# Kernel optimization log

Measured on AMD Instinct MI355X. Metric: run time of the kernel, lower is better.

Reference implementation:

```python
import jax, jax.numpy as jnp
import numpy as np

ATTN_DIM = 256


def setup_inputs() -> dict:
    key = jax.random.key(0)
    ks = jax.random.split(key, 10)
    B, Cu, Cj, H, W = 4, 320, 1024, 64, 64
    return {
        "unet_feat": jax.random.normal(ks[0], (B, Cu, H, W), jnp.float32),
        "janus_feat": jax.random.normal(ks[1], (B, Cj, H, W), jnp.float32),
        "Wq": jax.random.normal(ks[2], (ATTN_DIM, Cu), jnp.float32) * 0.02,
        "bq": jnp.zeros((ATTN_DIM,), jnp.float32),
        "Wk": jax.random.normal(ks[3], (ATTN_DIM, Cj), jnp.float32) * 0.02,
        "bk": jnp.zeros((ATTN_DIM,), jnp.float32),
        "Wv": jax.random.normal(ks[4], (Cu, Cj), jnp.float32) * 0.02,
        "bv": jnp.zeros((Cu,), jnp.float32),
        "Wo": jax.random.normal(ks[5], (Cu, Cu), jnp.float32) * 0.02,
        "bo": jnp.zeros((Cu,), jnp.float32),
    }


def reference(unet_feat, janus_feat, Wq, bq, Wk, bk, Wv, bv, Wo, bo):
    B, Cu, H, W = unet_feat.shape
    scale = ATTN_DIM ** (-0.5)
    # 1x1 convs == channel matmuls
    q = jnp.einsum('oc,bchw->bohw', Wq, unet_feat) + bq[None, :, None, None]
    k = jnp.einsum('oc,bchw->bohw', Wk, janus_feat) + bk[None, :, None, None]
    v = jnp.einsum('oc,bchw->bohw', Wv, janus_feat) + bv[None, :, None, None]
    N = H * W
    q = q.reshape(B, ATTN_DIM, N).transpose(0, 2, 1)  # [B, N, C]
    k = k.reshape(B, ATTN_DIM, N)                     # [B, C, N]
    v = v.reshape(B, Cu, N)                           # [B, Cu, N]
    attn = jax.nn.softmax(jnp.einsum('bic,bcj->bij', q, k) * scale, axis=-1)
    out = jnp.einsum('bcj,bij->bci', v, attn)         # [B, Cu, N]
    out = out.reshape(B, Cu, H, W)
    out = jnp.einsum('oc,bchw->bohw', Wo, out) + bo[None, :, None, None]
    return unet_feat + out
```

## Files before the change

kernel.cpp:

```cpp
#include <hip/hip_runtime.h>
#include <hip/hip_bf16.h>
#include <math.h>


typedef unsigned short u16;
typedef __attribute__((ext_vector_type(8))) short bf16x8;
typedef __attribute__((ext_vector_type(4))) float f32x4;
typedef __attribute__((ext_vector_type(16))) float f32x16;
typedef __attribute__((ext_vector_type(4))) unsigned short u16x4;

#define NB 4
#define CU 320
#define CJ 1024
#define NN 4096
#define AD 256

#define XU_OFF 0u
#define XJ_OFF 10485760u
#define QB_OFF 44040192u
#define KB_OFF 52428800u
#define VB_OFF 60817408u
#define WQ_OFF 71303168u
#define WK_OFF 71467008u
#define WV_OFF 71991296u
#define WO_OFF 72646656u
#define AO_OFF XU_OFF

__device__ __forceinline__ u16 f2b(float f) {
    union { float f; unsigned u; } v; v.f = f;
    unsigned u = v.u;
    unsigned r = (u + 0x7fffu + ((u >> 16) & 1u)) >> 16;
    return (u16)r;
}

__device__ __forceinline__ float b2f(u16 x) {
    union { unsigned u; float f; } v; v.u = ((unsigned)x) << 16;
    return v.f;
}

__device__ __forceinline__ unsigned cvt_pk_bf16(float lo, float hi) {
    unsigned r;
    asm("v_cvt_pk_bf16_f32 %0, %1, %2" : "=v"(r) : "v"(lo), "v"(hi));
    return r;
}

__device__ __forceinline__ float exp2_fast(float x) {
    float r;
    asm("v_exp_f32 %0, %1" : "=v"(r) : "v"(x));
    return r;
}

__device__ __forceinline__ void async_cp16(const u16* g, char* l) {
    __builtin_amdgcn_global_load_lds(
        (const __attribute__((address_space(1))) unsigned int*)g,
        (__attribute__((address_space(3))) unsigned int*)l, 16, 0, 0);
}

__global__ void wcast_kernel(const float* __restrict__ Wq, const float* __restrict__ Wk,
                             const float* __restrict__ Wv, const float* __restrict__ Wo,
                             u16* __restrict__ wq, u16* __restrict__ wk,
                             u16* __restrict__ wv, u16* __restrict__ wo) {
    int id = blockIdx.x * 256 + threadIdx.x;
    if (id < 81920) { wq[id] = f2b(Wq[id]); return; }
    id -= 81920;
    if (id < 262144) { wk[id] = f2b(Wk[id]); return; }
    id -= 262144;
    if (id < 327680) { wv[id] = f2b(Wv[id]); return; }
    id -= 327680;
    if (id < 102400) { wo[id] = f2b(Wo[id]); }
}

__global__ __launch_bounds__(256) void transpose_cast_kernel(
        const float* __restrict__ in, u16* __restrict__ out, int C, int Nn) {
    __shared__ float tile[64][65];
    int b = blockIdx.z;
    int n0 = blockIdx.x * 64, c0 = blockIdx.y * 64;
    const float* src = in + (size_t)b * C * Nn;
    u16* dst = out + (size_t)b * Nn * C;
    int t = threadIdx.x;
    int nl = t & 63, cl = t >> 6;
    #pragma unroll
    for (int k = 0; k < 16; ++k) {
        int c = cl + k * 4;
        tile[c][nl] = src[(size_t)(c0 + c) * Nn + n0 + nl];
    }
    __syncthreads();
    int cl2 = t & 63, nl2 = t >> 6;
    #pragma unroll
    for (int k = 0; k < 16; ++k) {
        int n = nl2 + k * 4;
        dst[(size_t)(n0 + n) * C + c0 + cl2] = f2b(tile[cl2][n]);
    }
}

template <int EPI, int KD, int NOUT>
__global__ __launch_bounds__(256, 2) void gemm_kernel(
        const u16* __restrict__ A, const u16* __restrict__ W,
        const float* __restrict__ bias, void* __restrict__ outp,
        const float* __restrict__ unet, float alpha) {
    __shared__ __align__(16) char smem[49152];
    const int t = threadIdx.x;
    const int lane = t & 63, wave = t >> 6;
    const int r = lane & 15, h = lane >> 4;
    const int wr = wave >> 1, wc = wave & 1;
    const int m0 = blockIdx.x * 128;
    const int bn0 = blockIdx.y * 64;

    int goffA[4], goffB[2];
    #pragma unroll
    for (int n = 0; n < 4; ++n) {
        int c = n * 256 + t;
        int row = c >> 3, s = c & 7;
        goffA[n] = (m0 + row) * KD + ((s ^ (row & 7)) << 3);
    }
    #pragma unroll
    for (int n = 0; n < 2; ++n) {
        int c = n * 256 + t;
        int row = c >> 3, s = c & 7;
        goffB[n] = (bn0 + row) * KD + ((s ^ (row & 7)) << 3);
    }
    const unsigned wb = (unsigned)(t & ~63) * 16u;

    #define GSTAGE(BUF, KT) do {                                                  \
        _Pragma("unroll")                                                         \
        for (int n_ = 0; n_ < 4; ++n_)                                            \
            async_cp16(A + goffA[n_] + (KT) * 64,                                 \
                       smem + (BUF) * 24576 + n_ * 4096 + wb);                    \
        _Pragma("unroll")                                                         \
        for (int n_ = 0; n_ < 2; ++n_)                                            \
            async_cp16(W + goffB[n_] + (KT) * 64,                                 \
                       smem + (BUF) * 24576 + 16384 + n_ * 4096 + wb);            \
    } while (0)

    f32x4 acc[4][2];
    #pragma unroll
    for (int fr = 0; fr < 4; ++fr)
        #pragma unroll
        for (int fc = 0; fc < 2; ++fc) acc[fr][fc] = (f32x4)0.0f;

    GSTAGE(0, 0);
    int buf = 0;
    const int KS = KD / 64;
    for (int kt = 0; kt < KS; ++kt) {
        if (kt < KS - 1) {
            GSTAGE(buf ^ 1, kt + 1);
            asm volatile("s_waitcnt vmcnt(6)" ::: "memory");
        } else {
            asm volatile("s_waitcnt vmcnt(0)" ::: "memory");
        }
        __builtin_amdgcn_s_barrier();
        asm volatile("" ::: "memory");
        const char* Ab = smem + buf * 24576;
        const char* Bb = smem + buf * 24576 + 16384;
        #pragma unroll
        for (int kk = 0; kk < 2; ++kk) {
            bf16x8 af[4], bf[2];
            #pragma unroll
            for (int fr = 0; fr < 4; ++fr) {
                int row = wr * 64 + fr * 16 + r;
                af[fr] = *(const bf16x8*)(Ab + row * 128 + (((kk * 4 + h) ^ (row & 7)) << 4));
            }
            #pragma unroll
            for (int fc = 0; fc < 2; ++fc) {
                int rowb = wc * 32 + fc * 16 + r;
                bf[fc] = *(const bf16x8*)(Bb + rowb * 128 + (((kk * 4 + h) ^ (rowb & 7)) << 4));
            }
            #pragma unroll
            for (int fr = 0; fr < 4; ++fr)
                #pragma unroll
                for (int fc = 0; fc < 2; ++fc)
                    acc[fr][fc] = __builtin_amdgcn_mfma_f32_16x16x32_bf16(
                        af[fr], bf[fc], acc[fr][fc], 0, 0, 0);
        }
        asm volatile("" ::: "memory");
        __builtin_amdgcn_s_barrier();
        asm volatile("" ::: "memory");
        buf ^= 1;
    }
    #undef GSTAGE

    const int mw = m0 + wr * 64;
    const int ob0 = bn0 + wc * 32;

    if (EPI == 0) {
        u16* out = (u16*)outp;
        #pragma unroll
        for (int fc = 0; fc < 2; ++fc) {
            int o = ob0 + fc * 16 + r;
            float bs = bias[o];
            #pragma unroll
            for (int fr = 0; fr < 4; ++fr)
                #pragma unroll
                for (int rr = 0; rr < 4; ++rr) {
                    int mrow = mw + fr * 16 + h * 4 + rr;
                    out[(size_t)mrow * NOUT + o] = f2b((acc[fr][fc][rr] + bs) * alpha);
                }
        }
    } else {
        float* tile = (float*)(smem + wave * 8704);
        #pragma unroll
        for (int fc = 0; fc < 2; ++fc)
            #pragma unroll
            for (int fr = 0; fr < 4; ++fr)
                *(f32x4*)(tile + (fc * 16 + r) * 68 + fr * 16 + h * 4) = acc[fr][fc];
        __builtin_amdgcn_s_waitcnt(0);
        float* out = (float*)outp;
        int bb = mw >> 12, nb = mw & 4095;
        #pragma unroll
        for (int g = 0; g < 8; ++g) {
            int chunk = g * 64 + lane;
            int row = chunk >> 4, ns = chunk & 15;
            int o = ob0 + row;
            size_t base = (size_t)bb * CU * NN + (size_t)o * NN + nb + ns * 4;
            f32x4 v = *(const f32x4*)(tile + row * 68 + ns * 4);
            f32x4 u = *(const f32x4*)(unet + base);
            float bs = bias[o];
            f32x4 res;
            #pragma unroll
            for (int rr = 0; rr < 4; ++rr) res[rr] = v[rr] + bs + u[rr];
            *(f32x4*)(out + base) = res;
        }
    }
}

__global__ __launch_bounds__(256, 2) void gemm_kv_kernel(
        const u16* __restrict__ A, const u16* __restrict__ Wk,
        const u16* __restrict__ Wv, const float* __restrict__ bk,
        const float* __restrict__ bv, u16* __restrict__ Kb,
        u16* __restrict__ Vb) {
    const int KD = 1024;
    __shared__ __align__(16) char smem[49152];
    const int t = threadIdx.x;
    const int lane = t & 63, wave = t >> 6;
    const int r = lane & 15, h = lane >> 4;
    const int wr = wave >> 1, wc = wave & 1;
    const int m0 = blockIdx.x * 128;
    const bool isK = blockIdx.y < 4;
    const int bn0 = (isK ? blockIdx.y : (blockIdx.y - 4)) * 64;
    const u16* W = isK ? Wk : Wv;
    const float* bias = isK ? bk : bv;

    int goffA[4], goffB[2];
    #pragma unroll
    for (int n = 0; n < 4; ++n) {
        int c = n * 256 + t;
        int row = c >> 3, s = c & 7;
        goffA[n] = (m0 + row) * KD + ((s ^ (row & 7)) << 3);
    }
    #pragma unroll
    for (int n = 0; n < 2; ++n) {
        int c = n * 256 + t;
        int row = c >> 3, s = c & 7;
        goffB[n] = (bn0 + row) * KD + ((s ^ (row & 7)) << 3);
    }
    const unsigned wb = (unsigned)(t & ~63) * 16u;

    #define GSTAGE(BUF, KT) do {                                                  \
        _Pragma("unroll")                                                         \
        for (int n_ = 0; n_ < 4; ++n_)                                            \
            async_cp16(A + goffA[n_] + (KT) * 64,                                 \
                       smem + (BUF) * 24576 + n_ * 4096 + wb);                    \
        _Pragma("unroll")                                                         \
        for (int n_ = 0; n_ < 2; ++n_)                                            \
            async_cp16(W + goffB[n_] + (KT) * 64,                                 \
                       smem + (BUF) * 24576 + 16384 + n_ * 4096 + wb);            \
    } while (0)

    f32x4 acc[4][2];
    #pragma unroll
    for (int fr = 0; fr < 4; ++fr)
        #pragma unroll
        for (int fc = 0; fc < 2; ++fc) acc[fr][fc] = (f32x4)0.0f;

    GSTAGE(0, 0);
    int buf = 0;
    for (int kt = 0; kt < 16; ++kt) {
        if (kt < 15) {
            GSTAGE(buf ^ 1, kt + 1);
            asm volatile("s_waitcnt vmcnt(6)" ::: "memory");
        } else {
            asm volatile("s_waitcnt vmcnt(0)" ::: "memory");
        }
        __builtin_amdgcn_s_barrier();
        asm volatile("" ::: "memory");
        const char* Ab = smem + buf * 24576;
        const char* Bb = smem + buf * 24576 + 16384;
        #pragma unroll
        for (int kk = 0; kk < 2; ++kk) {
            bf16x8 af[4], bf[2];
            #pragma unroll
            for (int fr = 0; fr < 4; ++fr) {
                int row = wr * 64 + fr * 16 + r;
                af[fr] = *(const bf16x8*)(Ab + row * 128 + (((kk * 4 + h) ^ (row & 7)) << 4));
            }
            #pragma unroll
            for (int fc = 0; fc < 2; ++fc) {
                int rowb = wc * 32 + fc * 16 + r;
                bf[fc] = *(const bf16x8*)(Bb + rowb * 128 + (((kk * 4 + h) ^ (rowb & 7)) << 4));
            }
            #pragma unroll
            for (int fr = 0; fr < 4; ++fr)
                #pragma unroll
                for (int fc = 0; fc < 2; ++fc)
                    acc[fr][fc] = __builtin_amdgcn_mfma_f32_16x16x32_bf16(
                        af[fr], bf[fc], acc[fr][fc], 0, 0, 0);
        }
        asm volatile("" ::: "memory");
        __builtin_amdgcn_s_barrier();
        asm volatile("" ::: "memory");
        buf ^= 1;
    }
    #undef GSTAGE

    const int mw = m0 + wr * 64;
    const int ob0 = bn0 + wc * 32;

    if (isK) {
        #pragma unroll
        for (int fc = 0; fc < 2; ++fc) {
            int o = ob0 + fc * 16 + r;
            float bs = bias[o];
            #pragma unroll
            for (int fr = 0; fr < 4; ++fr)
                #pragma unroll
                for (int rr = 0; rr < 4; ++rr) {
                    int mrow = mw + fr * 16 + h * 4 + rr;
                    Kb[(size_t)mrow * AD + o] = f2b((acc[fr][fc][rr] + bs));
                }
        }
    } else {
        u16* tile = (u16*)(smem + wave * 4608);
        #pragma unroll
        for (int fc = 0; fc < 2; ++fc) {
            int o = ob0 + fc * 16 + r;
            float bs = bias[o];
            #pragma unroll
            for (int fr = 0; fr < 4; ++fr) {
                u16x4 v4;
                #pragma unroll
                for (int rr = 0; rr < 4; ++rr) v4[rr] = f2b(acc[fr][fc][rr] + bs);
                *(u16x4*)(tile + (fc * 16 + r) * 72 + fr * 16 + h * 4) = v4;
            }
        }
        __builtin_amdgcn_s_waitcnt(0);
        int bb = mw >> 12, nb = mw & 4095;
        #pragma unroll
        for (int g = 0; g < 4; ++g) {
            int chunk = g * 64 + lane;
            int row = chunk >> 3, ns = chunk & 7;
            int ch = ob0 + row;
            int j = nb + ns * 8;
            bf16x8 val = *(const bf16x8*)(tile + row * 72 + ns * 8);
            size_t off = (size_t)bb * CU * NN + (size_t)(ch >> 5) * (NN * 32)
                       + (size_t)(j >> 4) * 512
                       + (size_t)((ch & 31) + ((j >> 3) & 1) * 32) * 8 + (j & 7);
            *(bf16x8*)(Vb + off) = val;
        }
    }
}

__global__ __launch_bounds__(768, 3) void attn_kernel(
        const u16* __restrict__ Q, const u16* __restrict__ K,
        const u16* __restrict__ V, u16* __restrict__ AO) {
    __shared__ __align__(16) char smem[84480];

    const int t = threadIdx.x;
    const int lane = t & 63;
    const int wave = t >> 6;
    const int r = lane & 31, hi = lane >> 5;

    int linear = blockIdx.x;
    int swz = (linear & 7) * 32 + (linear >> 3);
    int b = swz >> 6;
    int i0 = (swz & 63) * 64;

    const u16* Qb = Q + ((size_t)b * NN + i0) * AD;
    const u16* Kb = K + (size_t)b * NN * AD;
    const u16* Vb = V + (size_t)b * CU * NN;

    {
        #pragma unroll
        for (int n = 0; n < 2; ++n) {
            int id = n * 768 + t;
            int row = (id >> 5) & 63, c16 = id & 31;
            async_cp16(Kb + row * 256 + ((c16 ^ (row & 31)) << 3),
                       smem + (unsigned)(n * 768 + (t & ~63)) * 16u);
        }
        if (t < 512) {
            int id = 1536 + t;
            int row = (id >> 5) & 63, c16 = id & 31;
            async_cp16(Kb + row * 256 + ((c16 ^ (row & 31)) << 3),
                       smem + (unsigned)(1536 + (t & ~63)) * 16u);
        }
    }
    asm volatile("s_waitcnt vmcnt(0)" ::: "memory");
    __builtin_amdgcn_s_barrier();
    asm volatile("" ::: "memory");

    if (wave < 4) {
        const int iw = wave >> 1;
        const int jw = wave & 1;
        bf16x8 q[16];
        #pragma unroll
        for (int kk = 0; kk < 16; ++kk)
            q[kk] = *(const bf16x8*)(Qb + (size_t)(iw * 32 + r) * AD + kk * 16 + hi * 8);
        float m = -INFINITY, lsum = 0.0f;

        for (int i = 0; i < 64; ++i) {
            if (i) {
                __builtin_amdgcn_s_barrier();
                asm volatile("" ::: "memory");
            }
            const char* Kt = smem + (i & 1) * 32768 + jw * 16384;
            f32x16 sa = (f32x16)0.0f, sb = (f32x16)0.0f;
            __builtin_amdgcn_s_setprio(1);
            #pragma unroll
            for (int kk = 0; kk < 8; ++kk) {
                bf16x8 k0 = *(const bf16x8*)(Kt + r * 512 + (((2 * kk + hi) ^ r) << 4));
                bf16x8 k1 = *(const bf16x8*)(Kt + r * 512 + (((2 * (kk + 8) + hi) ^ r) << 4));
                sa = __builtin_amdgcn_mfma_f32_32x32x16_bf16(k0, q[kk], sa, 0, 0, 0);
                sb = __builtin_amdgcn_mfma_f32_32x32x16_bf16(k1, q[kk + 8], sb, 0, 0, 0);
            }
            __builtin_amdgcn_s_setprio(0);
            f32x16 s = sa + sb;

            float x0 = fmaxf(s[0], s[1]),   x1 = fmaxf(s[2], s[3]);
            float x2 = fmaxf(s[4], s[5]),   x3 = fmaxf(s[6], s[7]);
            float x4 = fmaxf(s[8], s[9]),   x5 = fmaxf(s[10], s[11]);
            float x6 = fmaxf(s[12], s[13]), x7 = fmaxf(s[14], s[15]);
            float pmax = fmaxf(fmaxf(fmaxf(x0, x1), fmaxf(x2, x3)),
                               fmaxf(fmaxf(x4, x5), fmaxf(x6, x7)));
            pmax = fmaxf(pmax, __shfl_xor(pmax, 32));
            char* pb = smem + 65536 + (i & 1) * 8960;
            int fl = __any(pmax > m + 8.0f) ? 1 : 0;
            if (fl) {
                float mn = fmaxf(m, pmax);
                float al = exp2_fast(m - mn);
                m = mn;
                lsum *= al;
                if (lane < 32) *(float*)(pb + 8192 + (iw * 2 + jw) * 128 + r * 4) = al;
            }
            if (lane == 0) *(int*)(pb + 8704 + (iw * 2 + jw) * 4) = fl;
            float p[16];
            #pragma unroll
            for (int e = 0; e < 16; ++e) p[e] = exp2_fast(s[e] - m);
            float y0 = (p[0] + p[1]) + (p[2] + p[3]);
            float y1 = (p[4] + p[5]) + (p[6] + p[7]);
            float y2 = (p[8] + p[9]) + (p[10] + p[11]);
            float y3 = (p[12] + p[13]) + (p[14] + p[15]);
            float ps = (y0 + y1) + (y2 + y3);
            ps += __shfl_xor(ps, 32);
            lsum += ps;

            #pragma unroll
            for (int ks = 0; ks < 2; ++ks) {
                unsigned a0 = cvt_pk_bf16(p[8 * ks + 0], p[8 * ks + 1]);
                unsigned a1 = cvt_pk_bf16(p[8 * ks + 2], p[8 * ks + 3]);
                unsigned b0 = cvt_pk_bf16(p[8 * ks + 4], p[8 * ks + 5]);
                unsigned b1 = cvt_pk_bf16(p[8 * ks + 6], p[8 * ks + 7]);
                asm("v_permlane32_swap_b32 %0, %1" : "+v"(a0), "+v"(b0));
                asm("v_permlane32_swap_b32 %0, %1" : "+v"(a1), "+v"(b1));
                union { unsigned w[4]; bf16x8 v; } u;
                u.w[0] = a0; u.w[1] = a1; u.w[2] = b0; u.w[3] = b1;
                *(bf16x8*)(pb + (iw * 2 + jw) * 2048 + ks * 1024 + lane * 16) = u.v;
            }
            asm volatile("s_waitcnt lgkmcnt(0)" ::: "memory");
            __builtin_amdgcn_sched_barrier(0);
        }
        __builtin_amdgcn_s_barrier();
        asm volatile("" ::: "memory");
        if (lane < 32) {
            *(float*)(smem + 83456 + (iw * 2 + jw) * 128 + r * 4) = m;
            *(float*)(smem + 83456 + 512 + (iw * 2 + jw) * 128 + r * 4) = lsum;
        }
        __syncthreads();
        __syncthreads();
        __syncthreads();
    } else {
        const int pvid = wave - 4;
        const int iw = pvid >> 2;
        const int pj = (pvid >> 1) & 1;
        const int cgh = pvid & 1;
        const int tp = t - 256;

        int goffp[4];
        #pragma unroll
        for (int n = 0; n < 4; ++n) {
            int id = n * 512 + tp;
            int row = (id >> 5) & 63;
            int c16 = id & 31;
            goffp[n] = row * 256 + ((c16 ^ (row & 31)) << 3);
        }
        const unsigned wbp = (unsigned)(tp & ~63) * 16u;

        #define STAGE(BUF, KP) do {                                               \
            _Pragma("unroll")                                                     \
            for (int n_ = 0; n_ < 4; ++n_)                                        \
                async_cp16((KP) + goffp[n_],                                      \
                           smem + (BUF) * 32768 + n_ * 8192 + wbp);               \
        } while (0)

        f32x16 o[5];
        #pragma unroll
        for (int ct = 0; ct < 5; ++ct) o[ct] = (f32x16)0.0f;
        const u16* vb = Vb + (size_t)(cgh * 5) * 131072 + lane * 8;

        #define PV_BODY(TI) do {                                                  \
            const char* pb = smem + 65536 + ((TI) & 1) * 8960;                    \
            int fl = *(volatile const int*)(pb + 8704 + (iw * 2 + pj) * 4);       \
            bf16x8 pf0 = *(const bf16x8*)(pb + (iw * 2 + pj) * 2048 + lane * 16); \
            bf16x8 pf1 = *(const bf16x8*)(pb + (iw * 2 + pj) * 2048 + 1024 +      \
                                          lane * 16);                             \
            bf16x8 vfA[5], vfB[5];                                                \
            _Pragma("unroll")                                                     \
            for (int c = 0; c < 5; ++c)                                           \
                vfA[c] = *(const bf16x8*)(vb + (size_t)c * 131072 +               \
                                          ((TI) * 4 + pj * 2 + 0) * 512);         \
            _Pragma("unroll")                                                     \
            for (int c = 0; c < 5; ++c)                                           \
                vfB[c] = *(const bf16x8*)(vb + (size_t)c * 131072 +               \
                                          ((TI) * 4 + pj * 2 + 1) * 512);         \
            if (fl) {                                                             \
                float alv = *(volatile const float*)(pb + 8192 +                  \
                                (iw * 2 + pj) * 128 + (lane & 31) * 4);           \
                _Pragma("unroll")                                                 \
                for (int ct = 0; ct < 5; ++ct) o[ct] *= alv;                      \
            }                                                                     \
            __builtin_amdgcn_s_setprio(1);                                        \
            _Pragma("unroll")                                                     \
            for (int ct = 0; ct < 5; ++ct)                                        \
                o[ct] = __builtin_amdgcn_mfma_f32_32x32x16_bf16(vfA[ct], pf0,     \
                                                                o[ct], 0, 0, 0); \
            _Pragma("unroll")                                                     \
            for (int ct = 0; ct < 5; ++ct)                                        \
                o[ct] = __builtin_amdgcn_mfma_f32_32x32x16_bf16(vfB[ct], pf1,     \
                                                                o[ct], 0, 0, 0); \
            __builtin_amdgcn_s_setprio(0);                                        \
        } while (0)

        for (int i = 0; i < 64; ++i) {
            if (i) {
                __builtin_amdgcn_s_barrier();
                asm volatile("" ::: "memory");
            }
            if (i < 63) STAGE((i + 1) & 1, Kb + (i + 1) * 16384);
            if (i >= 1) PV_BODY(i - 1);
            asm volatile("s_waitcnt vmcnt(0)" ::: "memory");
        }
        __builtin_amdgcn_s_barrier();
        asm volatile("" ::: "memory");
        PV_BODY(63);

        __syncthreads();
        float m0 = *(const float*)(smem + 83456 + (iw * 2 + pj) * 128 + r * 4);
        float l0 = *(const float*)(smem + 83456 + 512 + (iw * 2 + pj) * 128 + r * 4);
        float m1 = *(const float*)(smem + 83456 + (iw * 2 + (pj ^ 1)) * 128 + r * 4);
        float l1 = *(const float*)(smem + 83456 + 512 + (iw * 2 + (pj ^ 1)) * 128 + r * 4);
        float M = fmaxf(m0, m1);
        float fsc = exp2_fast(m0 - M);
        float fo = exp2_fast(m1 - M);
        float inv = 1.0f / (l0 * fsc + l1 * fo);

        u16* fb = (u16*)smem;
        if (pj == 1) {
            #pragma unroll
            for (int ct = 0; ct < 5; ++ct)
                #pragma unroll
                for (int e = 0; e < 16; ++e) {
                    int c = cgh * 160 + ct * 32 + (e & 3) + 8 * (e >> 2) + 4 * hi;
                    fb[(iw * 32 + r) * 328 + c] = f2b(o[ct][e] * fsc);
                }
        }
        __syncthreads();
        if (pj == 0) {
            #pragma unroll
            for (int ct = 0; ct < 5; ++ct)
                #pragma unroll
                for (int g = 0; g < 4; ++g) {
                    int cb = cgh * 160 + ct * 32 + 8 * g + 4 * hi;
                    u16* fr = &fb[(iw * 32 + r) * 328 + cb];
                    float v0 = (o[ct][4 * g + 0] * fsc + b2f(fr[0])) * inv;
                    float v1 = (o[ct][4 * g + 1] * fsc + b2f(fr[1])) * inv;
                    float v2 = (o[ct][4 * g + 2] * fsc + b2f(fr[2])) * inv;
                    float v3 = (o[ct][4 * g + 3] * fsc + b2f(fr[3])) * inv;
                    *(unsigned*)(fr) = cvt_pk_bf16(v0, v1);
                    *(unsigned*)(fr + 2) = cvt_pk_bf16(v2, v3);
                }
        }
        __syncthreads();
        #undef PV_BODY
        #undef STAGE
    }

    const u16* ob = (const u16*)smem;
    u16* AOb = AO + ((size_t)b * NN + i0) * CU;
    #pragma unroll
    for (int n = 0; n < 3; ++n) {
        int id = n * 768 + t;
        int row = id / 40, c8 = id % 40;
        bf16x8 val = *(const bf16x8*)(ob + row * 328 + c8 * 8);
        *(bf16x8*)(AOb + (size_t)row * CU + c8 * 8) = val;
    }
    if (t < 256) {
        int id = 2304 + t;
        int row = id / 40, c8 = id % 40;
        bf16x8 val = *(const bf16x8*)(ob + row * 328 + c8 * 8);
        *(bf16x8*)(AOb + (size_t)row * CU + c8 * 8) = val;
    }
}

extern "C" void kernel_launch(void* const* d_in, const int* in_sizes, int n_in,
                              void* d_out, int out_size, void* d_ws, size_t ws_size,
                              hipStream_t stream) {
    const float* unet  = (const float*)d_in[0];
    const float* janus = (const float*)d_in[1];
    const float* Wq = (const float*)d_in[2];
    const float* bq = (const float*)d_in[3];
    const float* Wk = (const float*)d_in[4];
    const float* bk = (const float*)d_in[5];
    const float* Wv = (const float*)d_in[6];
    const float* bv = (const float*)d_in[7];
    const float* Wo = (const float*)d_in[8];
    const float* bo = (const float*)d_in[9];
    float* out = (float*)d_out;

    char* ws = (char*)d_ws;
    u16* Xu  = (u16*)(ws + XU_OFF);
    u16* Xj  = (u16*)(ws + XJ_OFF);
    u16* Qb  = (u16*)(ws + QB_OFF);
    u16* Kb  = (u16*)(ws + KB_OFF);
    u16* Vb  = (u16*)(ws + VB_OFF);
    u16* wq  = (u16*)(ws + WQ_OFF);
    u16* wk  = (u16*)(ws + WK_OFF);
    u16* wv  = (u16*)(ws + WV_OFF);
    u16* wo  = (u16*)(ws + WO_OFF);
    u16* AO  = (u16*)(ws + AO_OFF);

    wcast_kernel<<<3024, 256, 0, stream>>>(Wq, Wk, Wv, Wo, wq, wk, wv, wo);

    transpose_cast_kernel<<<dim3(64, 5, NB), 256, 0, stream>>>(unet, Xu, CU, NN);
    transpose_cast_kernel<<<dim3(64, 16, NB), 256, 0, stream>>>(janus, Xj, CJ, NN);

    gemm_kernel<0, 320, 256><<<dim3(128, 4), 256, 0, stream>>>(
        Xu, wq, bq, Qb, nullptr, 0.0901684411f);

    gemm_kv_kernel<<<dim3(128, 9), 256, 0, stream>>>(
        Xj, wk, wv, bk, bv, Kb, Vb);

    attn_kernel<<<256, 768, 0, stream>>>(Qb, Kb, Vb, AO);

    gemm_kernel<2, 320, 320><<<dim3(128, 5), 256, 0, stream>>>(
        AO, wo, bo, out, unet, 1.0f);
}
```

Before: 183.7 us.

## Repartition attention PV waves to share V fragments across row tiles

The attention block grows from 12 to 14 waves, giving 10 PV waves instead of 8. Each PV wave now covers both 32-row query tiles and two 32-channel V tiles, rather than one row tile and five channel tiles. Each V fragment loaded from global memory then feeds two MFMAs, roughly halving per-block V load traffic and lowering accumulator registers per wave. The K staging, output copy and launch bounds are adjusted to the new thread count. In exchange, the extra waves add P fragment reads from LDS and scheduling pressure, and two waves sit idle during K staging.

```diff
diff --git a/kernel.cpp b/kernel.cpp
--- a/kernel.cpp
+++ b/kernel.cpp
@@ -359,7 +359,7 @@
     }
 }
 
-__global__ __launch_bounds__(768, 3) void attn_kernel(
+__global__ __launch_bounds__(896, 3) void attn_kernel(
         const u16* __restrict__ Q, const u16* __restrict__ K,
         const u16* __restrict__ V, u16* __restrict__ AO) {
     __shared__ __align__(16) char smem[84480];
@@ -381,16 +381,18 @@
     {
         #pragma unroll
         for (int n = 0; n < 2; ++n) {
-            int id = n * 768 + t;
+            int id = n * 896 + t;
+            if (id < 2048) {
+                int row = (id >> 5) & 63, c16 = id & 31;
+                async_cp16(Kb + row * 256 + ((c16 ^ (row & 31)) << 3),
+                           smem + (unsigned)(n * 896 + (t & ~63)) * 16u);
+            }
+        }
+        if (t < 256) {
+            int id = 1792 + t;
             int row = (id >> 5) & 63, c16 = id & 31;
             async_cp16(Kb + row * 256 + ((c16 ^ (row & 31)) << 3),
-                       smem + (unsigned)(n * 768 + (t & ~63)) * 16u);
-        }
-        if (t < 512) {
-            int id = 1536 + t;
-            int row = (id >> 5) & 63, c16 = id & 31;
-            async_cp16(Kb + row * 256 + ((c16 ^ (row & 31)) << 3),
-                       smem + (unsigned)(1536 + (t & ~63)) * 16u);
+                       smem + (unsigned)(1792 + (t & ~63)) * 16u);
         }
     }
     asm volatile("s_waitcnt vmcnt(0)" ::: "memory");
@@ -478,9 +480,8 @@
         __syncthreads();
     } else {
         const int pvid = wave - 4;
-        const int iw = pvid >> 2;
-        const int pj = (pvid >> 1) & 1;
-        const int cgh = pvid & 1;
+        const int pj = pvid / 5;
+        const int cg = pvid % 5;
         const int tp = t - 256;
 
         int goffp[4];
@@ -494,47 +495,56 @@
         const unsigned wbp = (unsigned)(tp & ~63) * 16u;
 
         #define STAGE(BUF, KP) do {                                               \
-            _Pragma("unroll")                                                     \
-            for (int n_ = 0; n_ < 4; ++n_)                                        \
-                async_cp16((KP) + goffp[n_],                                      \
-                           smem + (BUF) * 32768 + n_ * 8192 + wbp);               \
+            if (tp < 512) {                                                       \
+                _Pragma("unroll")                                                 \
+                for (int n_ = 0; n_ < 4; ++n_)                                    \
+                    async_cp16((KP) + goffp[n_],                                  \
+                               smem + (BUF) * 32768 + n_ * 8192 + wbp);           \
+            }                                                                     \
         } while (0)
 
-        f32x16 o[5];
-        #pragma unroll
-        for (int ct = 0; ct < 5; ++ct) o[ct] = (f32x16)0.0f;
-        const u16* vb = Vb + (size_t)(cgh * 5) * 131072 + lane * 8;
+        f32x16 o[2][2];
+        #pragma unroll
+        for (int iw = 0; iw < 2; ++iw)
+            #pragma unroll
+            for (int ct = 0; ct < 2; ++ct) o[iw][ct] = (f32x16)0.0f;
+        const u16* vb = Vb + (size_t)(cg * 2) * 131072 + lane * 8;
 
         #define PV_BODY(TI) do {                                                  \
             const char* pb = smem + 65536 + ((TI) & 1) * 8960;                    \
-            int fl = *(volatile const int*)(pb + 8704 + (iw * 2 + pj) * 4);       \
-            bf16x8 pf0 = *(const bf16x8*)(pb + (iw * 2 + pj) * 2048 + lane * 16); \
-            bf16x8 pf1 = *(const bf16x8*)(pb + (iw * 2 + pj) * 2048 + 1024 +      \
-                                          lane * 16);                             \
-            bf16x8 vfA[5], vfB[5];                                                \
-            _Pragma("unroll")                                                     \
-            for (int c = 0; c < 5; ++c)                                           \
-                vfA[c] = *(const bf16x8*)(vb + (size_t)c * 131072 +               \
+            int fl0 = *(volatile const int*)(pb + 8704 + (0 * 2 + pj) * 4);       \
+            int fl1 = *(volatile const int*)(pb + 8704 + (1 * 2 + pj) * 4);       \
+            bf16x8 pf00 = *(const bf16x8*)(pb + (0 * 2 + pj) * 2048 + lane * 16); \
+            bf16x8 pf01 = *(const bf16x8*)(pb + (0 * 2 + pj) * 2048 + 1024 +      \
+                                           lane * 16);                            \
+            bf16x8 pf10 = *(const bf16x8*)(pb + (1 * 2 + pj) * 2048 + lane * 16); \
+            bf16x8 pf11 = *(const bf16x8*)(pb + (1 * 2 + pj) * 2048 + 1024 +      \
+                                           lane * 16);                            \
+            bf16x8 v00 = *(const bf16x8*)(vb + ((TI) * 4 + pj * 2 + 0) * 512);    \
+            bf16x8 v01 = *(const bf16x8*)(vb + ((TI) * 4 + pj * 2 + 1) * 512);    \
+            bf16x8 v10 = *(const bf16x8*)(vb + 131072 +                           \
                                           ((TI) * 4 + pj * 2 + 0) * 512);         \
-            _Pragma("unroll")                                                     \
-            for (int c = 0; c < 5; ++c)                                           \
-                vfB[c] = *(const bf16x8*)(vb + (size_t)c * 131072 +               \
+            bf16x8 v11 = *(const bf16x8*)(vb + 131072 +                           \
                                           ((TI) * 4 + pj * 2 + 1) * 512);         \
-            if (fl) {                                                             \
+            if (fl0) {                                                            \
                 float alv = *(volatile const float*)(pb + 8192 +                  \
-                                (iw * 2 + pj) * 128 + (lane & 31) * 4);           \
-                _Pragma("unroll")                                                 \
-                for (int ct = 0; ct < 5; ++ct) o[ct] *= alv;                      \
+                                (0 * 2 + pj) * 128 + (lane & 31) * 4);            \
+                o[0][0] *= alv; o[0][1] *= alv;                                   \
+            }                                                                     \
+            if (fl1) {                                                            \
+                float alv = *(volatile const float*)(pb + 8192 +                  \
+                                (1 * 2 + pj) * 128 + (lane & 31) * 4);            \
+                o[1][0] *= alv; o[1][1] *= alv;                                   \
             }                                                                     \
             __builtin_amdgcn_s_setprio(1);                                        \
-            _Pragma("unroll")                                                     \
-            for (int ct = 0; ct < 5; ++ct)                                        \
-                o[ct] = __builtin_amdgcn_mfma_f32_32x32x16_bf16(vfA[ct], pf0,     \
-                                                                o[ct], 0, 0, 0); \
-            _Pragma("unroll")                                                     \
-            for (int ct = 0; ct < 5; ++ct)                                        \
-                o[ct] = __builtin_amdgcn_mfma_f32_32x32x16_bf16(vfB[ct], pf1,     \
-                                                                o[ct], 0, 0, 0); \
+            o[0][0] = __builtin_amdgcn_mfma_f32_32x32x16_bf16(v00, pf00, o[0][0], 0, 0, 0); \
+            o[0][1] = __builtin_amdgcn_mfma_f32_32x32x16_bf16(v10, pf00, o[0][1], 0, 0, 0); \
+            o[1][0] = __builtin_amdgcn_mfma_f32_32x32x16_bf16(v00, pf10, o[1][0], 0, 0, 0); \
+            o[1][1] = __builtin_amdgcn_mfma_f32_32x32x16_bf16(v10, pf10, o[1][1], 0, 0, 0); \
+            o[0][0] = __builtin_amdgcn_mfma_f32_32x32x16_bf16(v01, pf01, o[0][0], 0, 0, 0); \
+            o[0][1] = __builtin_amdgcn_mfma_f32_32x32x16_bf16(v11, pf01, o[0][1], 0, 0, 0); \
+            o[1][0] = __builtin_amdgcn_mfma_f32_32x32x16_bf16(v01, pf11, o[1][0], 0, 0, 0); \
+            o[1][1] = __builtin_amdgcn_mfma_f32_32x32x16_bf16(v11, pf11, o[1][1], 0, 0, 0); \
             __builtin_amdgcn_s_setprio(0);                                        \
         } while (0)
 
@@ -552,40 +562,49 @@
         PV_BODY(63);
 
         __syncthreads();
-        float m0 = *(const float*)(smem + 83456 + (iw * 2 + pj) * 128 + r * 4);
-        float l0 = *(const float*)(smem + 83456 + 512 + (iw * 2 + pj) * 128 + r * 4);
-        float m1 = *(const float*)(smem + 83456 + (iw * 2 + (pj ^ 1)) * 128 + r * 4);
-        float l1 = *(const float*)(smem + 83456 + 512 + (iw * 2 + (pj ^ 1)) * 128 + r * 4);
-        float M = fmaxf(m0, m1);
-        float fsc = exp2_fast(m0 - M);
-        float fo = exp2_fast(m1 - M);
-        float inv = 1.0f / (l0 * fsc + l1 * fo);
+        float fsc[2], inv[2];
+        #pragma unroll
+        for (int iw = 0; iw < 2; ++iw) {
+            float m0 = *(const float*)(smem + 83456 + (iw * 2 + pj) * 128 + r * 4);
+            float l0 = *(const float*)(smem + 83456 + 512 + (iw * 2 + pj) * 128 + r * 4);
+            float m1 = *(const float*)(smem + 83456 + (iw * 2 + (pj ^ 1)) * 128 + r * 4);
+            float l1 = *(const float*)(smem + 83456 + 512 + (iw * 2 + (pj ^ 1)) * 128 + r * 4);
+            float M = fmaxf(m0, m1);
+            float f0 = exp2_fast(m0 - M);
+            float f1 = exp2_fast(m1 - M);
+            fsc[iw] = f0;
+            inv[iw] = 1.0f / (l0 * f0 + l1 * f1);
+        }
 
         u16* fb = (u16*)smem;
         if (pj == 1) {
             #pragma unroll
-            for (int ct = 0; ct < 5; ++ct)
+            for (int iw = 0; iw < 2; ++iw)
                 #pragma unroll
-                for (int e = 0; e < 16; ++e) {
-                    int c = cgh * 160 + ct * 32 + (e & 3) + 8 * (e >> 2) + 4 * hi;
-                    fb[(iw * 32 + r) * 328 + c] = f2b(o[ct][e] * fsc);
-                }
+                for (int ct = 0; ct < 2; ++ct)
+                    #pragma unroll
+                    for (int e = 0; e < 16; ++e) {
+                        int c = cg * 64 + ct * 32 + (e & 3) + 8 * (e >> 2) + 4 * hi;
+                        fb[(iw * 32 + r) * 328 + c] = f2b(o[iw][ct][e] * fsc[iw]);
+                    }
         }
         __syncthreads();
         if (pj == 0) {
             #pragma unroll
-            for (int ct = 0; ct < 5; ++ct)
+            for (int iw = 0; iw < 2; ++iw)
                 #pragma unroll
-                for (int g = 0; g < 4; ++g) {
-                    int cb = cgh * 160 + ct * 32 + 8 * g + 4 * hi;
-                    u16* fr = &fb[(iw * 32 + r) * 328 + cb];
-                    float v0 = (o[ct][4 * g + 0] * fsc + b2f(fr[0])) * inv;
-                    float v1 = (o[ct][4 * g + 1] * fsc + b2f(fr[1])) * inv;
-                    float v2 = (o[ct][4 * g + 2] * fsc + b2f(fr[2])) * inv;
-                    float v3 = (o[ct][4 * g + 3] * fsc + b2f(fr[3])) * inv;
-                    *(unsigned*)(fr) = cvt_pk_bf16(v0, v1);
-                    *(unsigned*)(fr + 2) = cvt_pk_bf16(v2, v3);
-                }
+                for (int ct = 0; ct < 2; ++ct)
+                    #pragma unroll
+                    for (int g = 0; g < 4; ++g) {
+                        int cb = cg * 64 + ct * 32 + 8 * g + 4 * hi;
+                        u16* fr = &fb[(iw * 32 + r) * 328 + cb];
+                        float v0 = (o[iw][ct][4 * g + 0] * fsc[iw] + b2f(fr[0])) * inv[iw];
+                        float v1 = (o[iw][ct][4 * g + 1] * fsc[iw] + b2f(fr[1])) * inv[iw];
+                        float v2 = (o[iw][ct][4 * g + 2] * fsc[iw] + b2f(fr[2])) * inv[iw];
+                        float v3 = (o[iw][ct][4 * g + 3] * fsc[iw] + b2f(fr[3])) * inv[iw];
+                        *(unsigned*)(fr) = cvt_pk_bf16(v0, v1);
+                        *(unsigned*)(fr + 2) = cvt_pk_bf16(v2, v3);
+                    }
         }
         __syncthreads();
         #undef PV_BODY
@@ -595,14 +614,16 @@
     const u16* ob = (const u16*)smem;
     u16* AOb = AO + ((size_t)b * NN + i0) * CU;
     #pragma unroll
-    for (int n = 0; n < 3; ++n) {
-        int id = n * 768 + t;
-        int row = id / 40, c8 = id % 40;
-        bf16x8 val = *(const bf16x8*)(ob + row * 328 + c8 * 8);
-        *(bf16x8*)(AOb + (size_t)row * CU + c8 * 8) = val;
-    }
-    if (t < 256) {
-        int id = 2304 + t;
+    for (int n = 0; n < 2; ++n) {
+        int id = n * 896 + t;
+        if (id < 2560) {
+            int row = id / 40, c8 = id % 40;
+            bf16x8 val = *(const bf16x8*)(ob + row * 328 + c8 * 8);
+            *(bf16x8*)(AOb + (size_t)row * CU + c8 * 8) = val;
+        }
+    }
+    if (t < 768) {
+        int id = 1792 + t;
         int row = id / 40, c8 = id % 40;
         bf16x8 val = *(const bf16x8*)(ob + row * 328 + c8 * 8);
         *(bf16x8*)(AOb + (size_t)row * CU + c8 * 8) = val;
@@ -647,7 +668,7 @@
     gemm_kv_kernel<<<dim3(128, 9), 256, 0, stream>>>(
         Xj, wk, wv, bk, bv, Kb, Vb);
 
-    attn_kernel<<<256, 768, 0, stream>>>(Qb, Kb, Vb, AO);
+    attn_kernel<<<256, 896, 0, stream>>>(Qb, Kb, Vb, AO);
 
     gemm_kernel<2, 320, 320><<<dim3(128, 5), 256, 0, stream>>>(
         AO, wo, bo, out, unet, 1.0f);
```

Result: no change. 183.8 us (+0.1%).

## Merge prep kernels into one launch and enlarge GEMM tiles to 256 rows

Applied to the files above, without the earlier changes.

Folds the weight cast and both transpose-casts into a single prep kernel that dispatches on block index, removing two launches. The projection GEMMs now use 512-thread blocks covering 256 rows of M, sharing one B-tile load across twice as many A rows. This halves the grid and raises LDS use to 80 KB per block, which lowers occupancy and leaves fewer blocks to balance across CUs.

```diff
diff --git a/kernel.cpp b/kernel.cpp
--- a/kernel.cpp
+++ b/kernel.cpp
@@ -56,11 +56,46 @@
         (__attribute__((address_space(3))) unsigned int*)l, 16, 0, 0);
 }
 
-__global__ void wcast_kernel(const float* __restrict__ Wq, const float* __restrict__ Wk,
-                             const float* __restrict__ Wv, const float* __restrict__ Wo,
-                             u16* __restrict__ wq, u16* __restrict__ wk,
-                             u16* __restrict__ wv, u16* __restrict__ wo) {
-    int id = blockIdx.x * 256 + threadIdx.x;
+__global__ __launch_bounds__(256) void prep_kernel(
+        const float* __restrict__ unet, const float* __restrict__ janus,
+        const float* __restrict__ Wq, const float* __restrict__ Wk,
+        const float* __restrict__ Wv, const float* __restrict__ Wo,
+        u16* __restrict__ Xu, u16* __restrict__ Xj,
+        u16* __restrict__ wq, u16* __restrict__ wk,
+        u16* __restrict__ wv, u16* __restrict__ wo) {
+    __shared__ float tile[64][65];
+    int bid = blockIdx.x;
+    int t = threadIdx.x;
+
+    if (bid < 5376) {
+        const float* src;
+        u16* dst;
+        int C, x, y, z;
+        if (bid < 1280) {
+            z = bid / 320; int rem = bid % 320; y = rem / 64; x = rem % 64;
+            C = CU; src = unet + (size_t)z * CU * NN; dst = Xu + (size_t)z * NN * CU;
+        } else {
+            int idx = bid - 1280;
+            z = idx / 1024; int rem = idx % 1024; y = rem / 64; x = rem % 64;
+            C = CJ; src = janus + (size_t)z * CJ * NN; dst = Xj + (size_t)z * NN * CJ;
+        }
+        int n0 = x * 64, c0 = y * 64;
+        int nl = t & 63, cl = t >> 6;
+        #pragma unroll
+        for (int k = 0; k < 16; ++k) {
+            int c = cl + k * 4;
+            tile[c][nl] = src[(size_t)(c0 + c) * NN + n0 + nl];
+        }
+        __syncthreads();
+        int cl2 = t & 63, nl2 = t >> 6;
+        #pragma unroll
+        for (int k = 0; k < 16; ++k) {
+            int n = nl2 + k * 4;
+            dst[(size_t)(n0 + n) * C + c0 + cl2] = f2b(tile[cl2][n]);
+        }
+        return;
+    }
+    int id = (bid - 5376) * 256 + t;
     if (id < 81920) { wq[id] = f2b(Wq[id]); return; }
     id -= 81920;
     if (id < 262144) { wk[id] = f2b(Wk[id]); return; }
@@ -70,54 +105,29 @@
     if (id < 102400) { wo[id] = f2b(Wo[id]); }
 }
 
-__global__ __launch_bounds__(256) void transpose_cast_kernel(
-        const float* __restrict__ in, u16* __restrict__ out, int C, int Nn) {
-    __shared__ float tile[64][65];
-    int b = blockIdx.z;
-    int n0 = blockIdx.x * 64, c0 = blockIdx.y * 64;
-    const float* src = in + (size_t)b * C * Nn;
-    u16* dst = out + (size_t)b * Nn * C;
-    int t = threadIdx.x;
-    int nl = t & 63, cl = t >> 6;
-    #pragma unroll
-    for (int k = 0; k < 16; ++k) {
-        int c = cl + k * 4;
-        tile[c][nl] = src[(size_t)(c0 + c) * Nn + n0 + nl];
-    }
-    __syncthreads();
-    int cl2 = t & 63, nl2 = t >> 6;
-    #pragma unroll
-    for (int k = 0; k < 16; ++k) {
-        int n = nl2 + k * 4;
-        dst[(size_t)(n0 + n) * C + c0 + cl2] = f2b(tile[cl2][n]);
-    }
-}
-
 template <int EPI, int KD, int NOUT>
-__global__ __launch_bounds__(256, 2) void gemm_kernel(
+__global__ __launch_bounds__(512, 4) void gemm_kernel(
         const u16* __restrict__ A, const u16* __restrict__ W,
         const float* __restrict__ bias, void* __restrict__ outp,
         const float* __restrict__ unet, float alpha) {
-    __shared__ __align__(16) char smem[49152];
+    __shared__ __align__(16) char smem[81920];
     const int t = threadIdx.x;
     const int lane = t & 63, wave = t >> 6;
     const int r = lane & 15, h = lane >> 4;
     const int wr = wave >> 1, wc = wave & 1;
-    const int m0 = blockIdx.x * 128;
+    const int m0 = blockIdx.x * 256;
     const int bn0 = blockIdx.y * 64;
 
-    int goffA[4], goffB[2];
+    int goffA[4], goffB;
     #pragma unroll
     for (int n = 0; n < 4; ++n) {
-        int c = n * 256 + t;
+        int c = n * 512 + t;
         int row = c >> 3, s = c & 7;
         goffA[n] = (m0 + row) * KD + ((s ^ (row & 7)) << 3);
     }
-    #pragma unroll
-    for (int n = 0; n < 2; ++n) {
-        int c = n * 256 + t;
-        int row = c >> 3, s = c & 7;
-        goffB[n] = (bn0 + row) * KD + ((s ^ (row & 7)) << 3);
+    {
+        int row = t >> 3, s = t & 7;
+        goffB = (bn0 + row) * KD + ((s ^ (row & 7)) << 3);
     }
     const unsigned wb = (unsigned)(t & ~63) * 16u;
 
@@ -125,11 +135,9 @@
         _Pragma("unroll")                                                         \
         for (int n_ = 0; n_ < 4; ++n_)                                            \
             async_cp16(A + goffA[n_] + (KT) * 64,                                 \
-                       smem + (BUF) * 24576 + n_ * 4096 + wb);                    \
-        _Pragma("unroll")                                                         \
-        for (int n_ = 0; n_ < 2; ++n_)                                            \
-            async_cp16(W + goffB[n_] + (KT) * 64,                                 \
-                       smem + (BUF) * 24576 + 16384 + n_ * 4096 + wb);            \
+                       smem + (BUF) * 40960 + n_ * 8192 + wb);                    \
+        async_cp16(W + goffB + (KT) * 64,                                         \
+                   smem + (BUF) * 40960 + 32768 + wb);                            \
     } while (0)
 
     f32x4 acc[4][2];
@@ -144,14 +152,14 @@
     for (int kt = 0; kt < KS; ++kt) {
         if (kt < KS - 1) {
             GSTAGE(buf ^ 1, kt + 1);
-            asm volatile("s_waitcnt vmcnt(6)" ::: "memory");
+            asm volatile("s_waitcnt vmcnt(5)" ::: "memory");
         } else {
             asm volatile("s_waitcnt vmcnt(0)" ::: "memory");
         }
         __builtin_amdgcn_s_barrier();
         asm volatile("" ::: "memory");
-        const char* Ab = smem + buf * 24576;
-        const char* Bb = smem + buf * 24576 + 16384;
+        const char* Ab = smem + buf * 40960;
+        const char* Bb = smem + buf * 40960 + 32768;
         #pragma unroll
         for (int kk = 0; kk < 2; ++kk) {
             bf16x8 af[4], bf[2];
@@ -223,35 +231,33 @@
     }
 }
 
-__global__ __launch_bounds__(256, 2) void gemm_kv_kernel(
+__global__ __launch_bounds__(512, 4) void gemm_kv_kernel(
         const u16* __restrict__ A, const u16* __restrict__ Wk,
         const u16* __restrict__ Wv, const float* __restrict__ bk,
         const float* __restrict__ bv, u16* __restrict__ Kb,
         u16* __restrict__ Vb) {
     const int KD = 1024;
-    __shared__ __align__(16) char smem[49152];
+    __shared__ __align__(16) char smem[81920];
     const int t = threadIdx.x;
     const int lane = t & 63, wave = t >> 6;
     const int r = lane & 15, h = lane >> 4;
     const int wr = wave >> 1, wc = wave & 1;
-    const int m0 = blockIdx.x * 128;
+    const int m0 = blockIdx.x * 256;
     const bool isK = blockIdx.y < 4;
     const int bn0 = (isK ? blockIdx.y : (blockIdx.y - 4)) * 64;
     const u16* W = isK ? Wk : Wv;
     const float* bias = isK ? bk : bv;
 
-    int goffA[4], goffB[2];
+    int goffA[4], goffB;
     #pragma unroll
     for (int n = 0; n < 4; ++n) {
-        int c = n * 256 + t;
+        int c = n * 512 + t;
         int row = c >> 3, s = c & 7;
         goffA[n] = (m0 + row) * KD + ((s ^ (row & 7)) << 3);
     }
-    #pragma unroll
-    for (int n = 0; n < 2; ++n) {
-        int c = n * 256 + t;
-        int row = c >> 3, s = c & 7;
-        goffB[n] = (bn0 + row) * KD + ((s ^ (row & 7)) << 3);
+    {
+        int row = t >> 3, s = t & 7;
+        goffB = (bn0 + row) * KD + ((s ^ (row & 7)) << 3);
     }
     const unsigned wb = (unsigned)(t & ~63) * 16u;
 
@@ -259,11 +265,9 @@
         _Pragma("unroll")                                                         \
         for (int n_ = 0; n_ < 4; ++n_)                                            \
             async_cp16(A + goffA[n_] + (KT) * 64,                                 \
-                       smem + (BUF) * 24576 + n_ * 4096 + wb);                    \
-        _Pragma("unroll")                                                         \
-        for (int n_ = 0; n_ < 2; ++n_)                                            \
-            async_cp16(W + goffB[n_] + (KT) * 64,                                 \
-                       smem + (BUF) * 24576 + 16384 + n_ * 4096 + wb);            \
+                       smem + (BUF) * 40960 + n_ * 8192 + wb);                    \
+        async_cp16(W + goffB + (KT) * 64,                                         \
+                   smem + (BUF) * 40960 + 32768 + wb);                            \
     } while (0)
 
     f32x4 acc[4][2];
@@ -277,14 +281,14 @@
     for (int kt = 0; kt < 16; ++kt) {
         if (kt < 15) {
             GSTAGE(buf ^ 1, kt + 1);
-            asm volatile("s_waitcnt vmcnt(6)" ::: "memory");
+            asm volatile("s_waitcnt vmcnt(5)" ::: "memory");
         } else {
             asm volatile("s_waitcnt vmcnt(0)" ::: "memory");
         }
         __builtin_amdgcn_s_barrier();
         asm volatile("" ::: "memory");
-        const char* Ab = smem + buf * 24576;
-        const char* Bb = smem + buf * 24576 + 16384;
+        const char* Ab = smem + buf * 40960;
+        const char* Bb = smem + buf * 40960 + 32768;
         #pragma unroll
         for (int kk = 0; kk < 2; ++kk) {
             bf16x8 af[4], bf[2];
@@ -636,19 +640,17 @@
     u16* wo  = (u16*)(ws + WO_OFF);
     u16* AO  = (u16*)(ws + AO_OFF);
 
-    wcast_kernel<<<3024, 256, 0, stream>>>(Wq, Wk, Wv, Wo, wq, wk, wv, wo);
-
-    transpose_cast_kernel<<<dim3(64, 5, NB), 256, 0, stream>>>(unet, Xu, CU, NN);
-    transpose_cast_kernel<<<dim3(64, 16, NB), 256, 0, stream>>>(janus, Xj, CJ, NN);
-
-    gemm_kernel<0, 320, 256><<<dim3(128, 4), 256, 0, stream>>>(
+    prep_kernel<<<8400, 256, 0, stream>>>(unet, janus, Wq, Wk, Wv, Wo,
+                                          Xu, Xj, wq, wk, wv, wo);
+
+    gemm_kernel<0, 320, 256><<<dim3(64, 4), 512, 0, stream>>>(
         Xu, wq, bq, Qb, nullptr, 0.0901684411f);
 
-    gemm_kv_kernel<<<dim3(128, 9), 256, 0, stream>>>(
+    gemm_kv_kernel<<<dim3(64, 9), 512, 0, stream>>>(
         Xj, wk, wv, bk, bv, Kb, Vb);
 
     attn_kernel<<<256, 768, 0, stream>>>(Qb, Kb, Vb, AO);
 
-    gemm_kernel<2, 320, 320><<<dim3(128, 5), 256, 0, stream>>>(
+    gemm_kernel<2, 320, 320><<<dim3(64, 5), 512, 0, stream>>>(
         AO, wo, bo, out, unet, 1.0f);
 }
```

Result: no change. 182.6 us (-0.6%).
